# Optimization experiments

Measured on AMD Instinct MI355X. Metric: run time of the kernel, lower is better.

The kernel has to match this reference:

```python
import jax, jax.numpy as jnp
import numpy as np

KS = 3
PAD = 1


def setup_inputs() -> dict:
    key = jax.random.key(0)
    k1, k2, k3 = jax.random.split(key, 3)
    x = jax.random.normal(k1, (8, 64, 96, 96), dtype=jnp.float32)
    offset = jax.random.normal(k2, (8, 18, 96, 96), dtype=jnp.float32)
    W = jax.random.normal(k3, (64, 64, 3, 3), dtype=jnp.float32) * 0.05
    return {"x": x, "offset": offset, "W": W}


def _deform_conv(x, offset, W):
    ks, pad = KS, PAD
    b, c, H, Wd = x.shape
    N = offset.shape[1] // 2  # ks*ks
    h, w = offset.shape[2], offset.shape[3]
    xp = jnp.pad(x, ((0, 0), (0, 0), (pad, pad), (pad, pad)))
    hp, wp = H + 2 * pad, Wd + 2 * pad

    # p = p_0 + p_n + offset, permuted to [b, h, w, 2N]
    r = jnp.arange(-(ks - 1) // 2, (ks - 1) // 2 + 1)
    pn_x, pn_y = jnp.meshgrid(r, r, indexing="ij")
    p_n = jnp.concatenate([pn_x.ravel(), pn_y.ravel()]).reshape(1, 2 * N, 1, 1).astype(offset.dtype)
    p0x, p0y = jnp.meshgrid(jnp.arange(1, h + 1), jnp.arange(1, w + 1), indexing="ij")
    p_0 = jnp.concatenate(
        [jnp.broadcast_to(p0x[None, None], (1, N, h, w)),
         jnp.broadcast_to(p0y[None, None], (1, N, h, w))], axis=1
    ).astype(offset.dtype)
    p = jnp.transpose(p_0 + p_n + offset, (0, 2, 3, 1))  # [b,h,w,2N]
    px, py = p[..., :N], p[..., N:]

    fx, fy = jnp.floor(px), jnp.floor(py)
    q_lt_x = jnp.clip(fx, 0, hp - 1)
    q_lt_y = jnp.clip(fy, 0, wp - 1)
    q_rb_x = jnp.clip(fx + 1, 0, hp - 1)
    q_rb_y = jnp.clip(fy + 1, 0, wp - 1)

    # out-of-image mask (computed on unclamped p, as in original)
    mx = ((px < pad) | (px > hp - 1 - pad)).astype(px.dtype)
    my = ((py < pad) | (py > wp - 1 - pad)).astype(py.dtype)
    px = jnp.clip(px * (1 - mx) + fx * mx, 0, hp - 1)
    py = jnp.clip(py * (1 - my) + fy * my, 0, wp - 1)

    g_lt = (1 + (q_lt_x - px)) * (1 + (q_lt_y - py))
    g_rb = (1 - (q_rb_x - px)) * (1 - (q_rb_y - py))
    g_lb = (1 + (q_lt_x - px)) * (1 - (q_rb_y - py))
    g_rt = (1 - (q_rb_x - px)) * (1 + (q_lt_y - py))

    x_flat = xp.reshape(b, c, hp * wp)

    def gather(qx, qy):
        idx = (qx.astype(jnp.int32) * wp + qy.astype(jnp.int32)).reshape(b, -1)
        g = jax.vmap(lambda xf, ix: xf[:, ix])(x_flat, idx)
        return g.reshape(b, c, h, w, N)

    x_off = (g_lt[:, None] * gather(q_lt_x, q_lt_y)
             + g_rb[:, None] * gather(q_rb_x, q_rb_y)
             + g_lb[:, None] * gather(q_lt_x, q_rb_y)
             + g_rt[:, None] * gather(q_rb_x, q_lt_y))  # [b,c,h,w,N]

    # reshape: out[:,:, i*ks+ki, j*ks+kj] = x_off[:,:,i,j, ki*ks+kj]
    x_off = x_off.reshape(b, c, h, w, ks, ks)
    x_off = jnp.transpose(x_off, (0, 1, 2, 4, 3, 5)).reshape(b, c, h * ks, w * ks)

    return jax.lax.conv_general_dilated(
        x_off, W, window_strides=(ks, ks), padding="VALID",
        dimension_numbers=("NCHW", "OIHW", "NCHW"))


def reference(x, offset, W):
    return _deform_conv(x, offset, W)
```

## Files before the change

### kernel.cpp

```cpp
#include <hip/hip_runtime.h>


typedef __bf16 bf16_t;
typedef __bf16 bf16x8 __attribute__((ext_vector_type(8)));
typedef float  f32x4  __attribute__((ext_vector_type(4)));

#define NB 8
#define NC 64
#define NO 64
#define NH 96
#define NW 96
#define HP 98
#define NPT 9
#define PIX 64
#define ASTR 72

struct DCParams { int u0, u1, v0, v1; float glt, grb, glb, grt; };

__device__ __forceinline__ DCParams dc_params(const float* __restrict__ off, int b, int i, int j, int n) {
    const int a = n / 3, b2 = n % 3;
    const float offx = off[((size_t)(b * 18 + n) * NH + i) * NW + j];
    const float offy = off[((size_t)(b * 18 + 9 + n) * NH + i) * NW + j];
    float px = (float)(i + a) + offx;
    float py = (float)(j + b2) + offy;
    const float fx = floorf(px), fy = floorf(py);
    const float x0 = fminf(fmaxf(fx, 0.f), 97.f);
    const float x1 = fminf(fmaxf(fx + 1.f, 0.f), 97.f);
    const float y0 = fminf(fmaxf(fy, 0.f), 97.f);
    const float y1 = fminf(fmaxf(fy + 1.f, 0.f), 97.f);
    px = (px < 1.f || px > 96.f) ? x0 : px;
    py = (py < 1.f || py > 96.f) ? y0 : py;
    const float wx0 = 1.f + x0 - px;
    const float wx1 = 1.f - x1 + px;
    const float wy0 = 1.f + y0 - py;
    const float wy1 = 1.f - y1 + py;
    DCParams p;
    p.u0 = (int)x0; p.u1 = (int)x1; p.v0 = (int)y0; p.v1 = (int)y1;
    p.glt = wx0 * wy0; p.grb = wx1 * wy1; p.glb = wx0 * wy1; p.grt = wx1 * wy0;
    return p;
}

__global__ __launch_bounds__(256) void prep_all(const float* __restrict__ x, const float* __restrict__ W,
                                                bf16_t* __restrict__ xt, bf16_t* __restrict__ Bt) {
    __shared__ float tile[64][17];
    const int blk = blockIdx.x;
    const int b = blk & 7;
    const int r = blk >> 3;
    const int t = threadIdx.x;

    if (r < 576) {
        const int jt = r % 6;
        const int i  = r / 6;
        const int j0 = jt * 16;
        {
            const int jj = t & 15, cq = t >> 4;
            #pragma unroll
            for (int rr = 0; rr < 4; ++rr) {
                const int c = cq * 4 + rr;
                tile[c][jj] = x[(((size_t)b * NC + c) * NH + i) * NW + j0 + jj];
            }
        }
        __syncthreads();
        {
            const int c = t & 63, jq = t >> 6;
            #pragma unroll
            for (int rr = 0; rr < 4; ++rr) {
                const int jj = jq * 4 + rr;
                xt[(((size_t)b * HP + (i + 1)) * HP + (j0 + jj + 1)) * NC + c] = (bf16_t)tile[c][jj];
            }
        }
    } else if (r < 592) {
        const int idx = (r - 576) * 256 + t;
        uint4* xt4 = (uint4*)xt;
        const size_t ib = (size_t)b * (HP * HP * NC / 8);
        const uint4 z = {0, 0, 0, 0};
        if (idx < 1568) {
            const int u   = (idx < 784) ? 0 : 97;
            const int pos = (idx < 784) ? idx : idx - 784;
            xt4[ib + (size_t)u * 784 + pos] = z;
        } else if (idx < 3104) {
            const int k  = idx - 1568;
            const int v  = (k < 768) ? 0 : 97;
            const int kk = (k < 768) ? k : k - 768;
            const int u  = 1 + (kk >> 3), c8 = kk & 7;
            xt4[ib + (size_t)(u * HP + v) * 8 + c8] = z;
        }
    } else if (b == 0) {
        const int idx = (r - 592) * 256 + t;
        const int l = idx & 63, frag = idx >> 6;
        const int nt = frag & 3, kk = (frag >> 2) & 1, n = frag >> 3;
        const int o  = nt * 16 + (l & 15);
        const int cb = kk * 32 + 8 * (l >> 4);
        bf16x8 v;
        #pragma unroll
        for (int j = 0; j < 8; ++j)
            v[j] = (bf16_t)W[(size_t)o * 576 + (cb + j) * 9 + n];
        *(bf16x8*)(Bt + (size_t)idx * 8) = v;
    }
}

__device__ __forceinline__ void mfma_tap(const bf16_t* sAbuf, const bf16_t* __restrict__ Bt,
                                         int n, int w, int l, f32x4 acc[4]) {
    const int mrow = l & 15, khi = l >> 4;
    #pragma unroll
    for (int kk = 0; kk < 2; ++kk) {
        const bf16x8 bf = *(const bf16x8*)(Bt + (size_t)(((n * 2 + kk) * 4 + w)) * 512 + l * 8);
        #pragma unroll
        for (int mt = 0; mt < 4; ++mt) {
            const bf16x8 af = *(const bf16x8*)(sAbuf + (mt * 16 + mrow) * ASTR + kk * 32 + khi * 8);
            acc[mt] = __builtin_amdgcn_mfma_f32_16x16x32_bf16(af, bf, acc[mt], 0, 0, 0);
        }
    }
}

__global__ __launch_bounds__(256) void deform_mfma(const bf16_t* __restrict__ xt, const bf16_t* __restrict__ Bt,
                                                   const float* __restrict__ off, float* __restrict__ out) {
    __shared__ __align__(16) unsigned char smem[2 * PIX * ASTR * 2];
    bf16_t* sA = (bf16_t*)smem;
    float*  sO = (float*)smem;
    __shared__ __align__(16) int4   sI[2][PIX];
    __shared__ __align__(16) float4 sG[2][PIX];

    const int t = threadIdx.x;
    const int l = t & 63;
    const int w = t >> 6;
    const int bid = blockIdx.x;
    const int b  = bid & 7;
    const int pb = (bid >> 3) * PIX;

    const int pl   = l >> 3;
    const int slot = l & 7;
    const bf16_t* ibase = xt + (size_t)b * (HP * HP * NC) + slot * 8;

    f32x4 acc[4] = {};
    bf16x8 d[2][4];

    if (t < PIX) {
        const int pp = pb + t, ii = pp / 96, jj = pp - (pp / 96) * 96;
        const DCParams p = dc_params(off, b, ii, jj, 0);
        sI[0][t] = make_int4((p.u0 * HP + p.v0) * NC, (p.u1 * HP + p.v1) * NC,
                             (p.u0 * HP + p.v1) * NC, (p.u1 * HP + p.v0) * NC);
        sG[0][t] = make_float4(p.glt, p.grb, p.glb, p.grt);
    }
    __syncthreads();
    #pragma unroll
    for (int q = 0; q < 2; ++q) {
        const int px = w * 16 + pl + 8 * q;
        const int4 a4 = sI[0][px];
        d[q][0] = *(const bf16x8*)(ibase + a4.x);
        d[q][1] = *(const bf16x8*)(ibase + a4.y);
        d[q][2] = *(const bf16x8*)(ibase + a4.z);
        d[q][3] = *(const bf16x8*)(ibase + a4.w);
    }

    for (int n = 0; n < NPT; ++n) {
        bf16_t* buf = sA + (n & 1) * (PIX * ASTR);
        #pragma unroll
        for (int q = 0; q < 2; ++q) {
            const int px = w * 16 + pl + 8 * q;
            const float4 g = sG[n & 1][px];
            bf16x8 rv;
            #pragma unroll
            for (int e = 0; e < 8; ++e) {
                const float v = g.x * (float)d[q][0][e] + g.y * (float)d[q][1][e]
                              + g.z * (float)d[q][2][e] + g.w * (float)d[q][3][e];
                rv[e] = (bf16_t)v;
            }
            *(bf16x8*)(buf + px * ASTR + slot * 8) = rv;
        }
        if (n + 1 < NPT && t < PIX) {
            const int pp = pb + t, ii = pp / 96, jj = pp - (pp / 96) * 96;
            const DCParams p = dc_params(off, b, ii, jj, n + 1);
            sI[(n + 1) & 1][t] = make_int4((p.u0 * HP + p.v0) * NC, (p.u1 * HP + p.v1) * NC,
                                           (p.u0 * HP + p.v1) * NC, (p.u1 * HP + p.v0) * NC);
            sG[(n + 1) & 1][t] = make_float4(p.glt, p.grb, p.glb, p.grt);
        }
        __syncthreads();
        if (n + 1 < NPT) {
            #pragma unroll
            for (int q = 0; q < 2; ++q) {
                const int px = w * 16 + pl + 8 * q;
                const int4 a4 = sI[(n + 1) & 1][px];
                d[q][0] = *(const bf16x8*)(ibase + a4.x);
                d[q][1] = *(const bf16x8*)(ibase + a4.y);
                d[q][2] = *(const bf16x8*)(ibase + a4.z);
                d[q][3] = *(const bf16x8*)(ibase + a4.w);
            }
        }
        mfma_tap(buf, Bt, n, w, l, acc);
    }

    __syncthreads();

    const int orow = w * 16 + (l & 15);
    #pragma unroll
    for (int mt = 0; mt < 4; ++mt)
        #pragma unroll
        for (int r = 0; r < 4; ++r)
            sO[orow * 68 + mt * 16 + (l >> 4) * 4 + r] = acc[mt][r];
    __syncthreads();

    const int o = t >> 2, q = t & 3;
    float4* dst = (float4*)(out + ((size_t)(b * NO + o)) * (NH * NW) + pb + q * 16);
    const float* src = sO + o * 68 + q * 16;
    #pragma unroll
    for (int k2 = 0; k2 < 4; ++k2) dst[k2] = ((const float4*)src)[k2];
}

__global__ __launch_bounds__(256) void deform_naive(const float* __restrict__ x, const float* __restrict__ W,
                                                    const float* __restrict__ off, float* __restrict__ out) {
    __shared__ float sv[576];
    __shared__ DCParams sp[NPT];
    const int t = threadIdx.x;
    const int P = blockIdx.x;
    const int b = P / (NH * NW), pp = P - b * (NH * NW);
    const int i = pp / 96, j = pp - (pp / 96) * 96;
    if (t < NPT) sp[t] = dc_params(off, b, i, j, t);
    __syncthreads();
    for (int k = t; k < 576; k += 256) {
        const int c = k / 9, n = k - c * 9;
        const DCParams p = sp[n];
        const float* xb = x + ((size_t)(b * NC + c)) * (NH * NW);
        const float vlt = (p.u0 >= 1 && p.u0 <= 96 && p.v0 >= 1 && p.v0 <= 96) ? xb[(p.u0 - 1) * 96 + (p.v0 - 1)] : 0.f;
        const float vrb = (p.u1 >= 1 && p.u1 <= 96 && p.v1 >= 1 && p.v1 <= 96) ? xb[(p.u1 - 1) * 96 + (p.v1 - 1)] : 0.f;
        const float vlb = (p.u0 >= 1 && p.u0 <= 96 && p.v1 >= 1 && p.v1 <= 96) ? xb[(p.u0 - 1) * 96 + (p.v1 - 1)] : 0.f;
        const float vrt = (p.u1 >= 1 && p.u1 <= 96 && p.v0 >= 1 && p.v0 <= 96) ? xb[(p.u1 - 1) * 96 + (p.v0 - 1)] : 0.f;
        sv[k] = p.glt * vlt + p.grb * vrb + p.glb * vlb + p.grt * vrt;
    }
    __syncthreads();
    if (t < NO) {
        const float* wrow = W + (size_t)t * 576;
        float acc = 0.f;
        for (int k = 0; k < 576; ++k) acc += sv[k] * wrow[k];
        out[((size_t)(b * NO + t)) * (NH * NW) + pp] = acc;
    }
}

extern "C" void kernel_launch(void* const* d_in, const int* in_sizes, int n_in,
                              void* d_out, int out_size, void* d_ws, size_t ws_size,
                              hipStream_t stream) {
    const float* x   = (const float*)d_in[0];
    const float* off = (const float*)d_in[1];
    const float* W   = (const float*)d_in[2];
    float* out = (float*)d_out;

    const size_t XT_ELEMS = (size_t)NB * HP * HP * NC;
    const size_t XT_BYTES = XT_ELEMS * 2;
    const size_t BT_ELEMS = (size_t)NPT * NC * NO;
    const size_t need = XT_BYTES + BT_ELEMS * 2;

    if (ws_size >= need) {
        bf16_t* xt = (bf16_t*)d_ws;
        bf16_t* Bt = (bf16_t*)((char*)d_ws + XT_BYTES);
        prep_all<<<dim3(8 * 610), dim3(256), 0, stream>>>(x, W, xt, Bt);
        deform_mfma<<<dim3(NB * NH * NW / PIX), dim3(256), 0, stream>>>(xt, Bt, off, out);
    } else {
        deform_naive<<<dim3(NB * NH * NW), dim3(256), 0, stream>>>(x, W, off, out);
    }
}
```

Baseline: 38.24 us.

## Give each wave its own pixels to drop per-tap block barriers

The split across waves changes. Previously each wave owned 16 output channels over all 64 pixels. Now each wave owns 16 pixels across all 64 output channels, so its sampled A tile, offsets and bilinear weights are private to the wave. That removes the block-wide __syncthreads that ran on every tap, and the parameter computation becomes per wave. The cost is that each wave now loads four B fragments from global per k-step instead of one, and correctness relies on intra-wave LDS ordering.

After: 41.94 us. +9.7%, slower.

```diff
diff --git a/kernel.cpp b/kernel.cpp
--- a/kernel.cpp
+++ b/kernel.cpp
@@ -99,27 +99,13 @@
     }
 }
 
-__device__ __forceinline__ void mfma_tap(const bf16_t* sAbuf, const bf16_t* __restrict__ Bt,
-                                         int n, int w, int l, f32x4 acc[4]) {
-    const int mrow = l & 15, khi = l >> 4;
-    #pragma unroll
-    for (int kk = 0; kk < 2; ++kk) {
-        const bf16x8 bf = *(const bf16x8*)(Bt + (size_t)(((n * 2 + kk) * 4 + w)) * 512 + l * 8);
-        #pragma unroll
-        for (int mt = 0; mt < 4; ++mt) {
-            const bf16x8 af = *(const bf16x8*)(sAbuf + (mt * 16 + mrow) * ASTR + kk * 32 + khi * 8);
-            acc[mt] = __builtin_amdgcn_mfma_f32_16x16x32_bf16(af, bf, acc[mt], 0, 0, 0);
-        }
-    }
-}
-
 __global__ __launch_bounds__(256) void deform_mfma(const bf16_t* __restrict__ xt, const bf16_t* __restrict__ Bt,
                                                    const float* __restrict__ off, float* __restrict__ out) {
     __shared__ __align__(16) unsigned char smem[2 * PIX * ASTR * 2];
     bf16_t* sA = (bf16_t*)smem;
     float*  sO = (float*)smem;
-    __shared__ __align__(16) int4   sI[2][PIX];
-    __shared__ __align__(16) float4 sG[2][PIX];
+    __shared__ __align__(16) int4   sI[2][4][16];
+    __shared__ __align__(16) float4 sG[2][4][16];
 
     const int t = threadIdx.x;
     const int l = t & 63;
@@ -130,23 +116,26 @@
 
     const int pl   = l >> 3;
     const int slot = l & 7;
+    const int mrow = l & 15, khi = l >> 4;
     const bf16_t* ibase = xt + (size_t)b * (HP * HP * NC) + slot * 8;
 
     f32x4 acc[4] = {};
     bf16x8 d[2][4];
 
-    if (t < PIX) {
-        const int pp = pb + t, ii = pp / 96, jj = pp - (pp / 96) * 96;
-        const DCParams p = dc_params(off, b, ii, jj, 0);
-        sI[0][t] = make_int4((p.u0 * HP + p.v0) * NC, (p.u1 * HP + p.v1) * NC,
-                             (p.u0 * HP + p.v1) * NC, (p.u1 * HP + p.v0) * NC);
-        sG[0][t] = make_float4(p.glt, p.grb, p.glb, p.grt);
-    }
-    __syncthreads();
+    auto calc_params = [&](int n) {
+        if (l < 16) {
+            const int pp = pb + w * 16 + l, ii = pp / 96, jj = pp - (pp / 96) * 96;
+            const DCParams p = dc_params(off, b, ii, jj, n);
+            sI[n & 1][w][l] = make_int4((p.u0 * HP + p.v0) * NC, (p.u1 * HP + p.v1) * NC,
+                                        (p.u0 * HP + p.v1) * NC, (p.u1 * HP + p.v0) * NC);
+            sG[n & 1][w][l] = make_float4(p.glt, p.grb, p.glb, p.grt);
+        }
+    };
+
+    calc_params(0);
     #pragma unroll
     for (int q = 0; q < 2; ++q) {
-        const int px = w * 16 + pl + 8 * q;
-        const int4 a4 = sI[0][px];
+        const int4 a4 = sI[0][w][pl + 8 * q];
         d[q][0] = *(const bf16x8*)(ibase + a4.x);
         d[q][1] = *(const bf16x8*)(ibase + a4.y);
         d[q][2] = *(const bf16x8*)(ibase + a4.z);
@@ -157,8 +146,8 @@
         bf16_t* buf = sA + (n & 1) * (PIX * ASTR);
         #pragma unroll
         for (int q = 0; q < 2; ++q) {
-            const int px = w * 16 + pl + 8 * q;
-            const float4 g = sG[n & 1][px];
+            const int pxw = pl + 8 * q;
+            const float4 g = sG[n & 1][w][pxw];
             bf16x8 rv;
             #pragma unroll
             for (int e = 0; e < 8; ++e) {
@@ -166,38 +155,35 @@
                               + g.z * (float)d[q][2][e] + g.w * (float)d[q][3][e];
                 rv[e] = (bf16_t)v;
             }
-            *(bf16x8*)(buf + px * ASTR + slot * 8) = rv;
-        }
-        if (n + 1 < NPT && t < PIX) {
-            const int pp = pb + t, ii = pp / 96, jj = pp - (pp / 96) * 96;
-            const DCParams p = dc_params(off, b, ii, jj, n + 1);
-            sI[(n + 1) & 1][t] = make_int4((p.u0 * HP + p.v0) * NC, (p.u1 * HP + p.v1) * NC,
-                                           (p.u0 * HP + p.v1) * NC, (p.u1 * HP + p.v0) * NC);
-            sG[(n + 1) & 1][t] = make_float4(p.glt, p.grb, p.glb, p.grt);
-        }
-        __syncthreads();
+            *(bf16x8*)(buf + (w * 16 + pxw) * ASTR + slot * 8) = rv;
+        }
         if (n + 1 < NPT) {
+            calc_params(n + 1);
             #pragma unroll
             for (int q = 0; q < 2; ++q) {
-                const int px = w * 16 + pl + 8 * q;
-                const int4 a4 = sI[(n + 1) & 1][px];
+                const int4 a4 = sI[(n + 1) & 1][w][pl + 8 * q];
                 d[q][0] = *(const bf16x8*)(ibase + a4.x);
                 d[q][1] = *(const bf16x8*)(ibase + a4.y);
                 d[q][2] = *(const bf16x8*)(ibase + a4.z);
                 d[q][3] = *(const bf16x8*)(ibase + a4.w);
             }
         }
-        mfma_tap(buf, Bt, n, w, l, acc);
-    }
-
-    __syncthreads();
-
-    const int orow = w * 16 + (l & 15);
+        #pragma unroll
+        for (int kk = 0; kk < 2; ++kk) {
+            const bf16x8 af = *(const bf16x8*)(buf + (w * 16 + mrow) * ASTR + kk * 32 + khi * 8);
+            #pragma unroll
+            for (int nt = 0; nt < 4; ++nt) {
+                const bf16x8 bf = *(const bf16x8*)(Bt + (size_t)(((n * 2 + kk) * 4 + nt)) * 512 + l * 8);
+                acc[nt] = __builtin_amdgcn_mfma_f32_16x16x32_bf16(af, bf, acc[nt], 0, 0, 0);
+            }
+        }
+    }
+
+    __syncthreads();
+
     #pragma unroll
-    for (int mt = 0; mt < 4; ++mt)
-        #pragma unroll
-        for (int r = 0; r < 4; ++r)
-            sO[orow * 68 + mt * 16 + (l >> 4) * 4 + r] = acc[mt][r];
+    for (int nt = 0; nt < 4; ++nt)
+        *(f32x4*)(&sO[(nt * 16 + mrow) * 68 + w * 16 + khi * 4]) = acc[nt];
     __syncthreads();
 
     const int o = t >> 2, q = t & 3;
```

## Process deformable taps in pairs to halve barriers and deepen gather prefetch

Applied to the files above, without the earlier changes.

The tap loop now handles two kernel taps per iteration. Offset parameters for both taps are computed by 128 threads at once, and the bilinear gather loads for two taps are prefetched into registers. This halves the number of block-wide barriers and puts more global gathers in flight to hide latency. In exchange it doubles the gather registers and the shared-memory staging, which may reduce occupancy.

New measurement: 39.73 us. 3.9% more time.

```diff
diff --git a/kernel.cpp b/kernel.cpp
--- a/kernel.cpp
+++ b/kernel.cpp
@@ -14,6 +14,8 @@
 #define NPT 9
 #define PIX 64
 #define ASTR 72
+#define HALF (PIX * ASTR)
+#define SLOT (2 * HALF)
 
 struct DCParams { int u0, u1, v0, v1; float glt, grb, glb, grt; };
 
@@ -115,11 +117,11 @@
 
 __global__ __launch_bounds__(256) void deform_mfma(const bf16_t* __restrict__ xt, const bf16_t* __restrict__ Bt,
                                                    const float* __restrict__ off, float* __restrict__ out) {
-    __shared__ __align__(16) unsigned char smem[2 * PIX * ASTR * 2];
+    __shared__ __align__(16) unsigned char smem[SLOT * 2 * 2];
     bf16_t* sA = (bf16_t*)smem;
     float*  sO = (float*)smem;
-    __shared__ __align__(16) int4   sI[2][PIX];
-    __shared__ __align__(16) float4 sG[2][PIX];
+    __shared__ __align__(16) int4   sI[2][128];
+    __shared__ __align__(16) float4 sG[2][128];
 
     const int t = threadIdx.x;
     const int l = t & 63;
@@ -133,61 +135,70 @@
     const bf16_t* ibase = xt + (size_t)b * (HP * HP * NC) + slot * 8;
 
     f32x4 acc[4] = {};
-    bf16x8 d[2][4];
-
-    if (t < PIX) {
-        const int pp = pb + t, ii = pp / 96, jj = pp - (pp / 96) * 96;
-        const DCParams p = dc_params(off, b, ii, jj, 0);
-        sI[0][t] = make_int4((p.u0 * HP + p.v0) * NC, (p.u1 * HP + p.v1) * NC,
-                             (p.u0 * HP + p.v1) * NC, (p.u1 * HP + p.v0) * NC);
-        sG[0][t] = make_float4(p.glt, p.grb, p.glb, p.grt);
-    }
-    __syncthreads();
-    #pragma unroll
-    for (int q = 0; q < 2; ++q) {
-        const int px = w * 16 + pl + 8 * q;
-        const int4 a4 = sI[0][px];
-        d[q][0] = *(const bf16x8*)(ibase + a4.x);
-        d[q][1] = *(const bf16x8*)(ibase + a4.y);
-        d[q][2] = *(const bf16x8*)(ibase + a4.z);
-        d[q][3] = *(const bf16x8*)(ibase + a4.w);
-    }
-
-    for (int n = 0; n < NPT; ++n) {
-        bf16_t* buf = sA + (n & 1) * (PIX * ASTR);
-        #pragma unroll
-        for (int q = 0; q < 2; ++q) {
-            const int px = w * 16 + pl + 8 * q;
-            const float4 g = sG[n & 1][px];
-            bf16x8 rv;
-            #pragma unroll
-            for (int e = 0; e < 8; ++e) {
-                const float v = g.x * (float)d[q][0][e] + g.y * (float)d[q][1][e]
-                              + g.z * (float)d[q][2][e] + g.w * (float)d[q][3][e];
-                rv[e] = (bf16_t)v;
-            }
-            *(bf16x8*)(buf + px * ASTR + slot * 8) = rv;
-        }
-        if (n + 1 < NPT && t < PIX) {
-            const int pp = pb + t, ii = pp / 96, jj = pp - (pp / 96) * 96;
-            const DCParams p = dc_params(off, b, ii, jj, n + 1);
-            sI[(n + 1) & 1][t] = make_int4((p.u0 * HP + p.v0) * NC, (p.u1 * HP + p.v1) * NC,
-                                           (p.u0 * HP + p.v1) * NC, (p.u1 * HP + p.v0) * NC);
-            sG[(n + 1) & 1][t] = make_float4(p.glt, p.grb, p.glb, p.grt);
-        }
+    bf16x8 d[2][2][4];
+
+    auto params_pair = [&](int p) {
+        if (t < 128) {
+            const int tap = p * 2 + (t >> 6);
+            if (tap < NPT) {
+                const int pix = t & 63;
+                const int pp = pb + pix, ii = pp / 96, jj = pp - (pp / 96) * 96;
+                const DCParams pr = dc_params(off, b, ii, jj, tap);
+                sI[p & 1][t] = make_int4((pr.u0 * HP + pr.v0) * NC, (pr.u1 * HP + pr.v1) * NC,
+                                         (pr.u0 * HP + pr.v1) * NC, (pr.u1 * HP + pr.v0) * NC);
+                sG[p & 1][t] = make_float4(pr.glt, pr.grb, pr.glb, pr.grt);
+            }
+        }
+    };
+
+    auto gather_pair = [&](int p) {
+        #pragma unroll
+        for (int np = 0; np < 2; ++np) {
+            if (p * 2 + np < NPT) {
+                #pragma unroll
+                for (int q = 0; q < 2; ++q) {
+                    const int px = w * 16 + pl + 8 * q;
+                    const int4 a4 = sI[p & 1][(np << 6) | px];
+                    d[np][q][0] = *(const bf16x8*)(ibase + a4.x);
+                    d[np][q][1] = *(const bf16x8*)(ibase + a4.y);
+                    d[np][q][2] = *(const bf16x8*)(ibase + a4.z);
+                    d[np][q][3] = *(const bf16x8*)(ibase + a4.w);
+                }
+            }
+        }
+    };
+
+    params_pair(0);
+    __syncthreads();
+    gather_pair(0);
+
+    for (int p = 0; p < 5; ++p) {
+        bf16_t* buf = sA + (p & 1) * SLOT;
+        #pragma unroll
+        for (int np = 0; np < 2; ++np) {
+            if (p * 2 + np < NPT) {
+                #pragma unroll
+                for (int q = 0; q < 2; ++q) {
+                    const int px = w * 16 + pl + 8 * q;
+                    const float4 g = sG[p & 1][(np << 6) | px];
+                    bf16x8 rv;
+                    #pragma unroll
+                    for (int e = 0; e < 8; ++e) {
+                        const float v = g.x * (float)d[np][q][0][e] + g.y * (float)d[np][q][1][e]
+                                      + g.z * (float)d[np][q][2][e] + g.w * (float)d[np][q][3][e];
+                        rv[e] = (bf16_t)v;
+                    }
+                    *(bf16x8*)(buf + np * HALF + px * ASTR + slot * 8) = rv;
+                }
+            }
+        }
+        if (p + 1 < 5) params_pair(p + 1);
         __syncthreads();
-        if (n + 1 < NPT) {
-            #pragma unroll
-            for (int q = 0; q < 2; ++q) {
-                const int px = w * 16 + pl + 8 * q;
-                const int4 a4 = sI[(n + 1) & 1][px];
-                d[q][0] = *(const bf16x8*)(ibase + a4.x);
-                d[q][1] = *(const bf16x8*)(ibase + a4.y);
-                d[q][2] = *(const bf16x8*)(ibase + a4.z);
-                d[q][3] = *(const bf16x8*)(ibase + a4.w);
-            }
-        }
-        mfma_tap(buf, Bt, n, w, l, acc);
+        if (p + 1 < 5) gather_pair(p + 1);
+        #pragma unroll
+        for (int np = 0; np < 2; ++np)
+            if (p * 2 + np < NPT)
+                mfma_tap(buf + np * HALF, Bt, p * 2 + np, w, l, acc);
     }
 
     __syncthreads();
```
